# Performance work log

Hardware: AMD Instinct MI355X
Metric: run time of the kernel (lower is better)

## Reference

```python
import jax, jax.numpy as jnp
import numpy as np

NUM_HEADS = 16

def setup_inputs() -> dict:
    key = jax.random.key(0)
    k1, k2, k3 = jax.random.split(key, 3)
    B, S, D = 2, 2048, 1024
    x = jax.random.normal(k1, (B, S, D), dtype=jnp.float32)
    Wqkv = jax.random.normal(k2, (D, 3 * D), dtype=jnp.float32) * (1.0 / np.sqrt(D))
    bqkv = jnp.zeros((3 * D,), dtype=jnp.float32)
    Wo = jax.random.normal(k3, (D, D), dtype=jnp.float32) * (1.0 / np.sqrt(D))
    bo = jnp.zeros((D,), dtype=jnp.float32)
    return {"x": x, "Wqkv": Wqkv, "bqkv": bqkv, "Wo": Wo, "bo": bo}

def reference(x, Wqkv, bqkv, Wo, bo):
    B, S, D = x.shape
    H = NUM_HEADS
    hd = D // H
    # qkv projection, split into per-head q, k, v: [B, H, S, hd]
    qkv = (x @ Wqkv + bqkv).reshape(B, S, H, 3 * hd).transpose(0, 2, 1, 3)
    q, k, v = jnp.split(qkv, 3, axis=-1)
    # causal attention scores [B, H, S, S]
    scores = jnp.einsum('bhqd,bhkd->bhqk', q, k)
    causal = jnp.tril(jnp.ones((S, S), dtype=bool))  # True = keep
    scores = jnp.where(causal, scores, -jnp.inf)
    attn = jax.nn.softmax(scores / np.sqrt(hd).astype(np.float32), axis=-1)
    # dropout is identity in eval mode
    ctx = jnp.einsum('bhqk,bhkd->bhqd', attn, v)  # [B, H, S, hd]
    ctx = ctx.transpose(0, 2, 1, 3).reshape(B, S, D)
    return ctx @ Wo + bo
```

## Files before the change

### kernel.cpp

```cpp
#include <hip/hip_runtime.h>


typedef __attribute__((ext_vector_type(8))) __bf16 bf16x8;
typedef __attribute__((ext_vector_type(4))) float f32x4;
typedef __attribute__((ext_vector_type(4))) short short4v;

__device__ __forceinline__ unsigned short f2bf(float f) {
    union { float f; unsigned u; } v; v.f = f;
    unsigned r = v.u + 0x7fffu + ((v.u >> 16) & 1u);
    return (unsigned short)(r >> 16);
}

__device__ __forceinline__ unsigned pack_bf16x2_trunc(float a, float b) {
#if defined(__HIP_DEVICE_COMPILE__)
    return __builtin_amdgcn_perm(__builtin_bit_cast(unsigned, a),
                                 __builtin_bit_cast(unsigned, b), 0x03020706u);
#else
    return 0u;
#endif
}

__device__ __forceinline__ float fast_exp2(float x) {
#if defined(__HIP_DEVICE_COMPILE__)
    return __builtin_amdgcn_exp2f(x);
#else
    return x;
#endif
}

__device__ __forceinline__ void async_copy16(const unsigned short* g, unsigned short* l) {
    __builtin_amdgcn_global_load_lds(
        (const __attribute__((address_space(1))) unsigned int*)g,
        (__attribute__((address_space(3))) unsigned int*)l, 16, 0, 0);
}

__device__ __forceinline__ f32x4 mfma16x16x16(short4v a, short4v b, f32x4 c) {
#if defined(__HIP_DEVICE_COMPILE__)
    return __builtin_amdgcn_mfma_f32_16x16x16bf16_1k(a, b, c, 0, 0, 0);
#else
    return c;
#endif
}

__global__ __launch_bounds__(256) void convert_f32_bf16(
    const float* __restrict__ in, unsigned short* __restrict__ out)
{
    size_t i = ((size_t)blockIdx.x * 256 + threadIdx.x) * 8;
    float4 v0 = *(const float4*)(in + i);
    float4 v1 = *(const float4*)(in + i + 4);
    ushort4 a, b;
    a.x = f2bf(v0.x); a.y = f2bf(v0.y); a.z = f2bf(v0.z); a.w = f2bf(v0.w);
    b.x = f2bf(v1.x); b.y = f2bf(v1.y); b.z = f2bf(v1.z); b.w = f2bf(v1.w);
    *(ushort4*)(out + i) = a;
    *(ushort4*)(out + i + 4) = b;
}

__global__ __launch_bounds__(256) void transpose_f32_bf16(
    const float* __restrict__ in, unsigned short* __restrict__ out, int K, int N)
{
    __shared__ float T[64][65];
    const int tid = threadIdx.x;
    const int n0 = blockIdx.x * 64, k0 = blockIdx.y * 64;
#pragma unroll
    for (int i = 0; i < 4; i++) {
        int idx = tid + i * 256;
        int r = idx >> 4, c4 = (idx & 15) * 4;
        float4 v = *(const float4*)(in + (size_t)(k0 + r) * N + n0 + c4);
        T[r][c4 + 0] = v.x; T[r][c4 + 1] = v.y; T[r][c4 + 2] = v.z; T[r][c4 + 3] = v.w;
    }
    __syncthreads();
#pragma unroll
    for (int i = 0; i < 4; i++) {
        int idx = tid + i * 256;
        int n = idx >> 4, k4 = (idx & 15) * 4;
        ushort4 o;
        o.x = f2bf(T[k4 + 0][n]); o.y = f2bf(T[k4 + 1][n]);
        o.z = f2bf(T[k4 + 2][n]); o.w = f2bf(T[k4 + 3][n]);
        *(ushort4*)(out + (size_t)(n0 + n) * K + k0 + k4) = o;
    }
}

__global__ __launch_bounds__(256) void transpose_v(
    const unsigned short* __restrict__ vrow, unsigned short* __restrict__ vt)
{
    __shared__ unsigned short T[64 * 72];
    const int tid = threadIdx.x;
    const int bh = blockIdx.y;
    const int s0 = blockIdx.x * 64;
    const unsigned short* src = vrow + ((size_t)bh * 2048 + s0) * 64;
    unsigned short* dst = vt + (size_t)bh * 64 * 2048 + s0;
#pragma unroll
    for (int i = 0; i < 2; i++) {
        int idx = tid + i * 256;
        int s = idx >> 3, dg = (idx & 7) * 8;
        *(uint4*)&T[s * 72 + dg] = *(const uint4*)(src + s * 64 + dg);
    }
    __syncthreads();
#pragma unroll
    for (int i = 0; i < 2; i++) {
        int idx = tid + i * 256;
        int d = idx >> 3, sg = (idx & 7) * 8;
        ushort4 a, b;
        a.x = T[(sg + 0) * 72 + d]; a.y = T[(sg + 1) * 72 + d];
        a.z = T[(sg + 2) * 72 + d]; a.w = T[(sg + 3) * 72 + d];
        b.x = T[(sg + 4) * 72 + d]; b.y = T[(sg + 5) * 72 + d];
        b.z = T[(sg + 6) * 72 + d]; b.w = T[(sg + 7) * 72 + d];
        *(ushort4*)(dst + (size_t)d * 2048 + sg) = a;
        *(ushort4*)(dst + (size_t)d * 2048 + sg + 4) = b;
    }
}

__global__ __launch_bounds__(256) void gemm_qkv_bf(
    const unsigned short* __restrict__ Xbf,
    const unsigned short* __restrict__ WT,
    const float* __restrict__ bias,
    unsigned short* __restrict__ qws, unsigned short* __restrict__ kws,
    unsigned short* __restrict__ vrow)
{
    const int K = 1024;
    __shared__ __align__(16) unsigned short smem[128 * 136];
    unsigned short* As = smem;
    unsigned short* Bs = smem + 8192;
    const int tid = threadIdx.x;
    const int m0 = blockIdx.y * 128, n0 = blockIdx.x * 128;
    const int wave = tid >> 6, lane = tid & 63;
    const int wm = (wave >> 1) * 64, wn = (wave & 1) * 64;
    const int quad = lane >> 4, l16 = lane & 15;
    const int lrow = lane >> 3, lgrp = lane & 7;
    const int sg = lgrp ^ lrow;

    f32x4 acc[4][4];
    const f32x4 Z4 = {0.f, 0.f, 0.f, 0.f};
#pragma unroll
    for (int i = 0; i < 4; i++)
#pragma unroll
        for (int j = 0; j < 4; j++) acc[i][j] = Z4;

    for (int k0 = 0; k0 < K; k0 += 64) {
        __syncthreads();
#pragma unroll
        for (int c = 0; c < 4; c++) {
            int nb = (wave * 4 + c) * 8;
            async_copy16(Xbf + (size_t)(m0 + nb + lrow) * K + k0 + sg * 8, &As[nb * 64]);
            async_copy16(WT  + (size_t)(n0 + nb + lrow) * K + k0 + sg * 8, &Bs[nb * 64]);
        }
        __syncthreads();
#pragma unroll
        for (int kk = 0; kk < 2; kk++) {
            int pg = ((kk * 4 + quad) ^ (l16 & 7)) * 8;
            bf16x8 af[4], bfr[4];
#pragma unroll
            for (int mi = 0; mi < 4; mi++) af[mi] = *(const bf16x8*)&As[(wm + mi * 16 + l16) * 64 + pg];
#pragma unroll
            for (int ni = 0; ni < 4; ni++) bfr[ni] = *(const bf16x8*)&Bs[(wn + ni * 16 + l16) * 64 + pg];
#pragma unroll
            for (int mi = 0; mi < 4; mi++)
#pragma unroll
                for (int ni = 0; ni < 4; ni++)
                    acc[mi][ni] = __builtin_amdgcn_mfma_f32_16x16x32_bf16(af[mi], bfr[ni], acc[mi][ni], 0, 0, 0);
        }
    }
    __syncthreads();
#pragma unroll
    for (int ni = 0; ni < 4; ni++) {
        int colL = wn + ni * 16 + l16;
        int col = n0 + colL;
        int t = (col % 192) >> 6;
        float bv = bias[col];
        float scl = (t == 1) ? 0.18033688f : 1.0f;
#pragma unroll
        for (int mi = 0; mi < 4; mi++)
#pragma unroll
            for (int r = 0; r < 4; r++) {
                int row = wm + mi * 16 + quad * 4 + r;
                smem[row * 136 + colL] = f2bf((acc[mi][ni][r] + bv) * scl);
            }
    }
    __syncthreads();
#pragma unroll
    for (int i = 0; i < 8; i++) {
        int idx = tid + i * 256;
        int row = idx >> 4, g = idx & 15;
        int colL = g * 8;
        uint4 w = *(const uint4*)&smem[row * 136 + colL];
        int col = n0 + colL;
        int h = col / 192, rem = col % 192, t = rem >> 6, d = rem & 63;
        int grow = m0 + row;
        int b = grow >> 11, s = grow & 2047;
        unsigned short* dst = (t == 0) ? qws : (t == 1) ? kws : vrow;
        *(uint4*)(dst + ((size_t)(b * 16 + h) * 2048 + s) * 64 + d) = w;
    }
}

__device__ __constant__ unsigned ATTN_JOBS[47] = {
    16u | (0u<<8) | (17u<<16),
    15u | (0u<<8) | (16u<<16), 30u | (0u<<8) | (16u<<16), 31u | (0u<<8) | (16u<<16), 31u | (16u<<8) | (32u<<16),
    14u | (0u<<8) | (15u<<16), 28u | (0u<<8) | (15u<<16), 29u | (0u<<8) | (15u<<16), 29u | (15u<<8) | (30u<<16), 30u | (16u<<8) | (31u<<16),
    13u | (0u<<8) | (14u<<16), 26u | (0u<<8) | (14u<<16), 27u | (0u<<8) | (14u<<16), 27u | (14u<<8) | (28u<<16), 28u | (15u<<8) | (29u<<16),
    12u | (0u<<8) | (13u<<16), 24u | (0u<<8) | (13u<<16), 25u | (0u<<8) | (13u<<16), 25u | (13u<<8) | (26u<<16), 26u | (14u<<8) | (27u<<16),
    11u | (0u<<8) | (12u<<16), 22u | (0u<<8) | (12u<<16), 23u | (0u<<8) | (12u<<16), 23u | (12u<<8) | (24u<<16), 24u | (13u<<8) | (25u<<16),
    10u | (0u<<8) | (11u<<16), 20u | (0u<<8) | (11u<<16), 21u | (0u<<8) | (11u<<16), 21u | (11u<<8) | (22u<<16), 22u | (12u<<8) | (23u<<16),
     9u | (0u<<8) | (10u<<16), 18u | (0u<<8) | (10u<<16), 19u | (0u<<8) | (10u<<16), 19u | (10u<<8) | (20u<<16), 20u | (11u<<8) | (21u<<16),
     8u | (0u<<8) | ( 9u<<16), 17u | (0u<<8) | ( 9u<<16), 17u | ( 9u<<8) | (18u<<16), 18u | (10u<<8) | (19u<<16),
     7u | (0u<<8) | ( 8u<<16),  6u | (0u<<8) | ( 7u<<16),  5u | (0u<<8) | ( 6u<<16),  4u | (0u<<8) | ( 5u<<16),
     3u | (0u<<8) | ( 4u<<16),  2u | (0u<<8) | ( 3u<<16),  1u | (0u<<8) | ( 2u<<16),  0u | (0u<<8) | ( 1u<<16),
};

__global__ __launch_bounds__(128) void attn(
    const unsigned short* __restrict__ qws, const unsigned short* __restrict__ kws,
    const unsigned short* __restrict__ vtws, unsigned short* __restrict__ ctx,
    unsigned short* __restrict__ Opart, float* __restrict__ lpart)
{
    __shared__ __align__(16) unsigned short Qs[64 * 64];
    __shared__ __align__(16) unsigned short Ks[64 * 64];
    __shared__ __align__(16) unsigned short Vt[64][72];

    const int tid = threadIdx.x;
    const int wave = tid >> 6, lane = tid & 63, quad = lane >> 4, l16 = lane & 15;
    const int lrow = lane >> 3, lgrp = lane & 7;
    const int sg = lgrp ^ lrow;

    const unsigned job = ATTN_JOBS[blockIdx.x >> 5];
    const int bh = blockIdx.x & 31;
    const int tile = job & 0xff;
    const int js = (job >> 8) & 0xff, je = (job >> 16) & 0xff;
    const int q0 = tile * 64;
    const bool split = tile >= 17;

    const unsigned short* Q  = qws + (size_t)bh * 2048 * 64;
    const unsigned short* Kp = kws + (size_t)bh * 2048 * 64;
    const unsigned short* Vp = vtws + (size_t)bh * 64 * 2048;

#pragma unroll
    for (int c = 0; c < 4; c++) {
        int rb = (wave * 4 + c) * 8;
        async_copy16(Q + (size_t)(q0 + rb + lrow) * 64 + sg * 8, &Qs[rb * 64]);
    }

    const int wq = wave * 32;
    f32x4 o[4][2];
    const f32x4 Z4 = {0.f, 0.f, 0.f, 0.f};
#pragma unroll
    for (int dt = 0; dt < 4; dt++)
#pragma unroll
        for (int qt = 0; qt < 2; qt++) o[dt][qt] = Z4;
    float lsum[2] = {0.f, 0.f};

    for (int j = js; j < je; j++) {
        const int kb0 = j * 64;
        __syncthreads();
#pragma unroll
        for (int c = 0; c < 4; c++) {
            int rb = (wave * 4 + c) * 8;
            async_copy16(Kp + (size_t)(kb0 + rb + lrow) * 64 + sg * 8, &Ks[rb * 64]);
        }
#pragma unroll
        for (int ii = 0; ii < 4; ii++) {
            int id2 = tid + ii * 128;
            int row = id2 >> 3, c = (id2 & 7) * 8;
            *(uint4*)&Vt[row][c] = *(const uint4*)(Vp + (size_t)row * 2048 + kb0 + c);
        }
        __syncthreads();

        if (kb0 <= q0 + wq + 31) {
            f32x4 sc[4][2];
#pragma unroll
            for (int kt = 0; kt < 4; kt++)
#pragma unroll
                for (int qt = 0; qt < 2; qt++) sc[kt][qt] = Z4;
#pragma unroll
            for (int kk = 0; kk < 2; kk++) {
                int pg = ((kk * 4 + quad) ^ (l16 & 7)) * 8;
                bf16x8 ak[4], bq[2];
#pragma unroll
                for (int kt = 0; kt < 4; kt++) ak[kt] = *(const bf16x8*)&Ks[(kt * 16 + l16) * 64 + pg];
#pragma unroll
                for (int qt = 0; qt < 2; qt++) bq[qt] = *(const bf16x8*)&Qs[(wq + qt * 16 + l16) * 64 + pg];
#pragma unroll
                for (int kt = 0; kt < 4; kt++)
#pragma unroll
                    for (int qt = 0; qt < 2; qt++)
                        sc[kt][qt] = __builtin_amdgcn_mfma_f32_16x16x32_bf16(ak[kt], bq[qt], sc[kt][qt], 0, 0, 0);
            }
            short4v pb[4][2];
            if (kb0 + 63 <= q0 + wq) {
#pragma unroll
                for (int qt = 0; qt < 2; qt++)
#pragma unroll
                    for (int kt = 0; kt < 4; kt++) {
                        float p0 = fast_exp2(sc[kt][qt][0]);
                        float p1 = fast_exp2(sc[kt][qt][1]);
                        float p2 = fast_exp2(sc[kt][qt][2]);
                        float p3 = fast_exp2(sc[kt][qt][3]);
                        lsum[qt] += (p0 + p1) + (p2 + p3);
                        uint2 uu;
                        uu.x = pack_bf16x2_trunc(p0, p1);
                        uu.y = pack_bf16x2_trunc(p2, p3);
                        pb[kt][qt] = __builtin_bit_cast(short4v, uu);
                    }
            } else {
#pragma unroll
                for (int qt = 0; qt < 2; qt++) {
                    int qg = q0 + wq + qt * 16 + l16;
#pragma unroll
                    for (int kt = 0; kt < 4; kt++) {
                        float p[4];
#pragma unroll
                        for (int r = 0; r < 4; r++) {
                            int key = kb0 + kt * 16 + quad * 4 + r;
                            float t = fast_exp2(sc[kt][qt][r]);
                            p[r] = (key <= qg) ? t : 0.f;
                        }
                        lsum[qt] += (p[0] + p[1]) + (p[2] + p[3]);
                        uint2 uu;
                        uu.x = pack_bf16x2_trunc(p[0], p[1]);
                        uu.y = pack_bf16x2_trunc(p[2], p[3]);
                        pb[kt][qt] = __builtin_bit_cast(short4v, uu);
                    }
                }
            }
#pragma unroll
            for (int kt = 0; kt < 4; kt++) {
#pragma unroll
                for (int dt = 0; dt < 4; dt++) {
                    short4v av = *(const short4v*)&Vt[dt * 16 + l16][kt * 16 + quad * 4];
#pragma unroll
                    for (int qt = 0; qt < 2; qt++)
                        o[dt][qt] = mfma16x16x16(av, pb[kt][qt], o[dt][qt]);
                }
            }
        }
    }
#pragma unroll
    for (int qt = 0; qt < 2; qt++) {
        lsum[qt] += __shfl_xor(lsum[qt], 16);
        lsum[qt] += __shfl_xor(lsum[qt], 32);
    }
    if (!split) {
        const int b = bh >> 4, h = bh & 15;
#pragma unroll
        for (int qt = 0; qt < 2; qt++) {
            int qg = q0 + wq + qt * 16 + l16;
            float inv = 1.0f / lsum[qt];
#pragma unroll
            for (int dt = 0; dt < 4; dt++) {
                ushort4 ov;
                ov.x = f2bf(o[dt][qt][0] * inv);
                ov.y = f2bf(o[dt][qt][1] * inv);
                ov.z = f2bf(o[dt][qt][2] * inv);
                ov.w = f2bf(o[dt][qt][3] * inv);
                *(ushort4*)(ctx + (size_t)(b * 2048 + qg) * 1024 + h * 64 + dt * 16 + quad * 4) = ov;
            }
        }
    } else {
        const int chunk = (js > 0) ? 1 : 0;
        const size_t slot = (size_t)bh * 30 + (tile - 17) * 2 + chunk;
        unsigned short* ob = Opart + slot * 4096;
#pragma unroll
        for (int qt = 0; qt < 2; qt++) {
            int rl = wq + qt * 16 + l16;
#pragma unroll
            for (int dt = 0; dt < 4; dt++) {
                ushort4 ov;
                ov.x = f2bf(o[dt][qt][0]);
                ov.y = f2bf(o[dt][qt][1]);
                ov.z = f2bf(o[dt][qt][2]);
                ov.w = f2bf(o[dt][qt][3]);
                *(ushort4*)(ob + (size_t)rl * 64 + dt * 16 + quad * 4) = ov;
            }
            if (quad == 0) lpart[slot * 64 + rl] = lsum[qt];
        }
    }
}

__global__ __launch_bounds__(256) void attn_combine(
    const unsigned short* __restrict__ Opart, const float* __restrict__ lpart,
    unsigned short* __restrict__ ctx)
{
    const int t = 17 + blockIdx.x;
    const int bh = blockIdx.y;
    const int tid = threadIdx.x;
    const int row = tid >> 2, dg = (tid & 3) * 16;
    const size_t s0 = (size_t)bh * 30 + (t - 17) * 2;
    const float inv = 1.0f / (lpart[s0 * 64 + row] + lpart[(s0 + 1) * 64 + row]);
    const unsigned short* p1 = Opart + s0 * 4096 + (size_t)row * 64 + dg;
    const unsigned short* p2 = p1 + 4096;
    const int b = bh >> 4, h = bh & 15;
    unsigned short* dst = ctx + ((size_t)(b * 2048 + t * 64 + row)) * 1024 + h * 64 + dg;
#pragma unroll
    for (int g = 0; g < 2; g++) {
        ushort a1[8], a2[8], ov[8];
        *(uint4*)a1 = *(const uint4*)(p1 + g * 8);
        *(uint4*)a2 = *(const uint4*)(p2 + g * 8);
#pragma unroll
        for (int e = 0; e < 8; e++) {
            float f1 = __builtin_bit_cast(float, (unsigned)a1[e] << 16);
            float f2 = __builtin_bit_cast(float, (unsigned)a2[e] << 16);
            ov[e] = f2bf((f1 + f2) * inv);
        }
        *(uint4*)(dst + g * 8) = *(const uint4*)ov;
    }
}

__global__ __launch_bounds__(256) void gemm_out(
    const unsigned short* __restrict__ Ctx, const unsigned short* __restrict__ WT,
    const float* __restrict__ bias, float* __restrict__ Out)
{
    const int K = 1024, N = 1024;
    __shared__ __align__(16) unsigned short As[64 * 64];
    __shared__ __align__(16) unsigned short Bs[128 * 64];
    const int tid = threadIdx.x;
    const int m0 = blockIdx.y * 64, n0 = blockIdx.x * 128;
    const int wave = tid >> 6, lane = tid & 63;
    const int wm = (wave >> 1) * 32, wn = (wave & 1) * 64;
    const int quad = lane >> 4, l16 = lane & 15;
    const int lrow = lane >> 3, lgrp = lane & 7;
    const int sg = lgrp ^ lrow;

    f32x4 acc[2][4];
    const f32x4 Z4 = {0.f, 0.f, 0.f, 0.f};
#pragma unroll
    for (int i = 0; i < 2; i++)
#pragma unroll
        for (int j = 0; j < 4; j++) acc[i][j] = Z4;

    for (int k0 = 0; k0 < K; k0 += 64) {
        __syncthreads();
#pragma unroll
        for (int c = 0; c < 2; c++) {
            int nb = (wave * 2 + c) * 8;
            async_copy16(Ctx + (size_t)(m0 + nb + lrow) * K + k0 + sg * 8, &As[nb * 64]);
        }
#pragma unroll
        for (int c = 0; c < 4; c++) {
            int nb = (wave * 4 + c) * 8;
            async_copy16(WT + (size_t)(n0 + nb + lrow) * K + k0 + sg * 8, &Bs[nb * 64]);
        }
        __syncthreads();
#pragma unroll
        for (int kk = 0; kk < 2; kk++) {
            int pg = ((kk * 4 + quad) ^ (l16 & 7)) * 8;
            bf16x8 af[2], bfr[4];
#pragma unroll
            for (int mi = 0; mi < 2; mi++) af[mi] = *(const bf16x8*)&As[(wm + mi * 16 + l16) * 64 + pg];
#pragma unroll
            for (int ni = 0; ni < 4; ni++) bfr[ni] = *(const bf16x8*)&Bs[(wn + ni * 16 + l16) * 64 + pg];
#pragma unroll
            for (int mi = 0; mi < 2; mi++)
#pragma unroll
                for (int ni = 0; ni < 4; ni++)
                    acc[mi][ni] = __builtin_amdgcn_mfma_f32_16x16x32_bf16(af[mi], bfr[ni], acc[mi][ni], 0, 0, 0);
        }
    }
#pragma unroll
    for (int mi = 0; mi < 2; mi++)
#pragma unroll
        for (int ni = 0; ni < 4; ni++) {
            int col = n0 + wn + ni * 16 + l16;
            float bv = bias[col];
#pragma unroll
            for (int r = 0; r < 4; r++) {
                int row = m0 + wm + mi * 16 + quad * 4 + r;
                Out[(size_t)row * N + col] = acc[mi][ni][r] + bv;
            }
        }
}

extern "C" void kernel_launch(void* const* d_in, const int* in_sizes, int n_in,
                              void* d_out, int out_size, void* d_ws, size_t ws_size,
                              hipStream_t stream) {
    const float* x    = (const float*)d_in[0];
    const float* Wqkv = (const float*)d_in[1];
    const float* bqkv = (const float*)d_in[2];
    const float* Wo   = (const float*)d_in[3];
    const float* bo   = (const float*)d_in[4];
    float* out = (float*)d_out;

    const size_t R = 4194304;
    unsigned short* q    = (unsigned short*)d_ws;
    unsigned short* k    = q + R;
    unsigned short* vrow = k + R;
    unsigned short* ctx  = vrow + R;
    unsigned short* xbf  = ctx + R;
    unsigned short* vt   = xbf;
    unsigned short* wqkvT = ctx;
    unsigned short* woT   = q;
    unsigned short* Opart = vrow;
    float* lpart = (float*)(vrow + 960 * (size_t)4096);

    convert_f32_bf16<<<dim3(2048), 256, 0, stream>>>(x, xbf);
    transpose_f32_bf16<<<dim3(48, 16), 256, 0, stream>>>(Wqkv, wqkvT, 1024, 3072);
    gemm_qkv_bf<<<dim3(24, 32), 256, 0, stream>>>(xbf, wqkvT, bqkv, q, k, vrow);
    transpose_v<<<dim3(32, 32), 256, 0, stream>>>(vrow, vt);
    attn<<<dim3(1504), 128, 0, stream>>>(q, k, vt, ctx, Opart, lpart);
    attn_combine<<<dim3(15, 32), 256, 0, stream>>>(Opart, lpart, ctx);
    transpose_f32_bf16<<<dim3(16, 16), 256, 0, stream>>>(Wo, woT, 1024, 1024);
    gemm_out<<<dim3(8, 64), 256, 0, stream>>>(ctx, woT, bo, out);
}
```

Measured before the change: 197.4 us.

## Fuse x fp32-to-bf16 conversion into QKV GEMM and rebalance split-KV attention jobs

Drops the separate conversion kernel: the QKV GEMM now loads fp32 x directly, converts it to bf16 in registers and writes it into swizzled LDS, while the weights still use async global-to-LDS copies. The attention job table is rebuilt so causal query tiles from 12 upward are split into two or three KV chunks. Chunk 0 writes straight into ctx and the combine kernel reads it back, which reduces Opart traffic. In exchange, the GEMM A-tile loads become synchronous and occupy VGPRs, and the combine kernel gains a read-modify-write of ctx.

Measured after the change: 208.0 us. +5.4%, slower.

```diff
diff --git a/kernel.cpp b/kernel.cpp
--- a/kernel.cpp
+++ b/kernel.cpp
@@ -9,6 +9,10 @@
     union { float f; unsigned u; } v; v.f = f;
     unsigned r = v.u + 0x7fffu + ((v.u >> 16) & 1u);
     return (unsigned short)(r >> 16);
+}
+
+__device__ __forceinline__ float bf2f(unsigned short u) {
+    return __builtin_bit_cast(float, (unsigned)u << 16);
 }
 
 __device__ __forceinline__ unsigned pack_bf16x2_trunc(float a, float b) {
@@ -40,19 +44,6 @@
 #else
     return c;
 #endif
-}
-
-__global__ __launch_bounds__(256) void convert_f32_bf16(
-    const float* __restrict__ in, unsigned short* __restrict__ out)
-{
-    size_t i = ((size_t)blockIdx.x * 256 + threadIdx.x) * 8;
-    float4 v0 = *(const float4*)(in + i);
-    float4 v1 = *(const float4*)(in + i + 4);
-    ushort4 a, b;
-    a.x = f2bf(v0.x); a.y = f2bf(v0.y); a.z = f2bf(v0.z); a.w = f2bf(v0.w);
-    b.x = f2bf(v1.x); b.y = f2bf(v1.y); b.z = f2bf(v1.z); b.w = f2bf(v1.w);
-    *(ushort4*)(out + i) = a;
-    *(ushort4*)(out + i + 4) = b;
 }
 
 __global__ __launch_bounds__(256) void transpose_f32_bf16(
@@ -110,8 +101,8 @@
     }
 }
 
-__global__ __launch_bounds__(256) void gemm_qkv_bf(
-    const unsigned short* __restrict__ Xbf,
+__global__ __launch_bounds__(256) void gemm_qkv(
+    const float* __restrict__ X,
     const unsigned short* __restrict__ WT,
     const float* __restrict__ bias,
     unsigned short* __restrict__ qws, unsigned short* __restrict__ kws,
@@ -141,8 +132,21 @@
 #pragma unroll
         for (int c = 0; c < 4; c++) {
             int nb = (wave * 4 + c) * 8;
-            async_copy16(Xbf + (size_t)(m0 + nb + lrow) * K + k0 + sg * 8, &As[nb * 64]);
-            async_copy16(WT  + (size_t)(n0 + nb + lrow) * K + k0 + sg * 8, &Bs[nb * 64]);
+            async_copy16(WT + (size_t)(n0 + nb + lrow) * K + k0 + sg * 8, &Bs[nb * 64]);
+        }
+#pragma unroll
+        for (int i = 0; i < 4; i++) {
+            int idx = tid + i * 256;
+            int m = idx >> 3, g = idx & 7;
+            const float* xp = X + (size_t)(m0 + m) * K + k0 + g * 8;
+            float4 v0 = *(const float4*)xp;
+            float4 v1 = *(const float4*)(xp + 4);
+            ushort4 a, b;
+            a.x = f2bf(v0.x); a.y = f2bf(v0.y); a.z = f2bf(v0.z); a.w = f2bf(v0.w);
+            b.x = f2bf(v1.x); b.y = f2bf(v1.y); b.z = f2bf(v1.z); b.w = f2bf(v1.w);
+            int pg = g ^ (m & 7);
+            *(ushort4*)&As[m * 64 + pg * 8] = a;
+            *(ushort4*)&As[m * 64 + pg * 8 + 4] = b;
         }
         __syncthreads();
 #pragma unroll
@@ -192,19 +196,26 @@
     }
 }
 
-__device__ __constant__ unsigned ATTN_JOBS[47] = {
-    16u | (0u<<8) | (17u<<16),
-    15u | (0u<<8) | (16u<<16), 30u | (0u<<8) | (16u<<16), 31u | (0u<<8) | (16u<<16), 31u | (16u<<8) | (32u<<16),
-    14u | (0u<<8) | (15u<<16), 28u | (0u<<8) | (15u<<16), 29u | (0u<<8) | (15u<<16), 29u | (15u<<8) | (30u<<16), 30u | (16u<<8) | (31u<<16),
-    13u | (0u<<8) | (14u<<16), 26u | (0u<<8) | (14u<<16), 27u | (0u<<8) | (14u<<16), 27u | (14u<<8) | (28u<<16), 28u | (15u<<8) | (29u<<16),
-    12u | (0u<<8) | (13u<<16), 24u | (0u<<8) | (13u<<16), 25u | (0u<<8) | (13u<<16), 25u | (13u<<8) | (26u<<16), 26u | (14u<<8) | (27u<<16),
-    11u | (0u<<8) | (12u<<16), 22u | (0u<<8) | (12u<<16), 23u | (0u<<8) | (12u<<16), 23u | (12u<<8) | (24u<<16), 24u | (13u<<8) | (25u<<16),
-    10u | (0u<<8) | (11u<<16), 20u | (0u<<8) | (11u<<16), 21u | (0u<<8) | (11u<<16), 21u | (11u<<8) | (22u<<16), 22u | (12u<<8) | (23u<<16),
-     9u | (0u<<8) | (10u<<16), 18u | (0u<<8) | (10u<<16), 19u | (0u<<8) | (10u<<16), 19u | (10u<<8) | (20u<<16), 20u | (11u<<8) | (21u<<16),
-     8u | (0u<<8) | ( 9u<<16), 17u | (0u<<8) | ( 9u<<16), 17u | ( 9u<<8) | (18u<<16), 18u | (10u<<8) | (19u<<16),
-     7u | (0u<<8) | ( 8u<<16),  6u | (0u<<8) | ( 7u<<16),  5u | (0u<<8) | ( 6u<<16),  4u | (0u<<8) | ( 5u<<16),
-     3u | (0u<<8) | ( 4u<<16),  2u | (0u<<8) | ( 3u<<16),  1u | (0u<<8) | ( 2u<<16),  0u | (0u<<8) | ( 1u<<16),
+#define J(t, s, e, c) ((unsigned)(t) | ((unsigned)(s) << 8) | ((unsigned)(e) << 16) | ((unsigned)(c) << 24))
+__device__ __constant__ unsigned ATTN_JOBS[60] = {
+    J(22,0,12,0), J(23,0,12,0), J(23,12,24,1), J(11,0,12,0),
+    J(20,0,11,0), J(21,0,11,0), J(21,11,22,1), J(22,12,23,1),
+    J(30,0,11,0), J(31,0,11,0), J(31,11,22,1), J(10,0,11,0),
+    J(18,0,10,0), J(19,0,10,0), J(19,10,20,1), J(20,11,21,1),
+    J(27,0,10,0), J(28,0,10,0), J(28,10,20,1), J(29,0,10,0),
+    J(29,10,20,1), J(29,20,30,2), J(30,11,21,1), J(30,21,31,2),
+    J(31,22,32,2), J(9,0,10,0),
+    J(16,0,9,0), J(17,0,9,0), J(17,9,18,1), J(18,10,19,1),
+    J(24,0,9,0), J(25,0,9,0), J(25,9,18,1), J(26,0,9,0),
+    J(26,9,18,1), J(26,18,27,2), J(27,10,19,1), J(27,19,28,2),
+    J(28,20,29,2), J(8,0,9,0),
+    J(14,0,8,0), J(15,0,8,0), J(15,8,16,1), J(16,9,17,1),
+    J(24,9,17,1), J(24,17,25,2), J(25,18,26,2), J(7,0,8,0),
+    J(12,0,7,0), J(13,0,7,0), J(13,7,14,1), J(14,8,15,1), J(6,0,7,0),
+    J(12,7,13,1), J(5,0,6,0), J(4,0,5,0), J(3,0,4,0), J(2,0,3,0),
+    J(1,0,2,0), J(0,0,1,0),
 };
+#undef J
 
 __global__ __launch_bounds__(128) void attn(
     const unsigned short* __restrict__ qws, const unsigned short* __restrict__ kws,
@@ -224,8 +235,9 @@
     const int bh = blockIdx.x & 31;
     const int tile = job & 0xff;
     const int js = (job >> 8) & 0xff, je = (job >> 16) & 0xff;
+    const int chunk = (job >> 24) & 0xff;
     const int q0 = tile * 64;
-    const bool split = tile >= 17;
+    const bool split = tile >= 12;
 
     const unsigned short* Q  = qws + (size_t)bh * 2048 * 64;
     const unsigned short* Kp = kws + (size_t)bh * 2048 * 64;
@@ -336,8 +348,8 @@
         lsum[qt] += __shfl_xor(lsum[qt], 16);
         lsum[qt] += __shfl_xor(lsum[qt], 32);
     }
+    const int b = bh >> 4, h = bh & 15;
     if (!split) {
-        const int b = bh >> 4, h = bh & 15;
 #pragma unroll
         for (int qt = 0; qt < 2; qt++) {
             int qg = q0 + wq + qt * 16 + l16;
@@ -353,22 +365,45 @@
             }
         }
     } else {
-        const int chunk = (js > 0) ? 1 : 0;
-        const size_t slot = (size_t)bh * 30 + (tile - 17) * 2 + chunk;
-        unsigned short* ob = Opart + slot * 4096;
+        const int ls = (tile < 24) ? (tile - 12) * 2 + chunk
+                                   : 24 + (tile - 24) * 3 + chunk;
+        float* lp = lpart + ((size_t)bh * 48 + ls) * 64;
 #pragma unroll
         for (int qt = 0; qt < 2; qt++) {
             int rl = wq + qt * 16 + l16;
-#pragma unroll
-            for (int dt = 0; dt < 4; dt++) {
-                ushort4 ov;
-                ov.x = f2bf(o[dt][qt][0]);
-                ov.y = f2bf(o[dt][qt][1]);
-                ov.z = f2bf(o[dt][qt][2]);
-                ov.w = f2bf(o[dt][qt][3]);
-                *(ushort4*)(ob + (size_t)rl * 64 + dt * 16 + quad * 4) = ov;
-            }
-            if (quad == 0) lpart[slot * 64 + rl] = lsum[qt];
+            if (quad == 0) lp[rl] = lsum[qt];
+        }
+        if (chunk == 0) {
+#pragma unroll
+            for (int qt = 0; qt < 2; qt++) {
+                int qg = q0 + wq + qt * 16 + l16;
+#pragma unroll
+                for (int dt = 0; dt < 4; dt++) {
+                    ushort4 ov;
+                    ov.x = f2bf(o[dt][qt][0]);
+                    ov.y = f2bf(o[dt][qt][1]);
+                    ov.z = f2bf(o[dt][qt][2]);
+                    ov.w = f2bf(o[dt][qt][3]);
+                    *(ushort4*)(ctx + (size_t)(b * 2048 + qg) * 1024 + h * 64 + dt * 16 + quad * 4) = ov;
+                }
+            }
+        } else {
+            const int os = (tile < 24) ? (tile - 12)
+                                       : 12 + (tile - 24) * 2 + (chunk - 1);
+            unsigned short* ob = Opart + ((size_t)bh * 28 + os) * 4096;
+#pragma unroll
+            for (int qt = 0; qt < 2; qt++) {
+                int rl = wq + qt * 16 + l16;
+#pragma unroll
+                for (int dt = 0; dt < 4; dt++) {
+                    ushort4 ov;
+                    ov.x = f2bf(o[dt][qt][0]);
+                    ov.y = f2bf(o[dt][qt][1]);
+                    ov.z = f2bf(o[dt][qt][2]);
+                    ov.w = f2bf(o[dt][qt][3]);
+                    *(ushort4*)(ob + (size_t)rl * 64 + dt * 16 + quad * 4) = ov;
+                }
+            }
         }
     }
 }
@@ -377,26 +412,31 @@
     const unsigned short* __restrict__ Opart, const float* __restrict__ lpart,
     unsigned short* __restrict__ ctx)
 {
-    const int t = 17 + blockIdx.x;
+    const int t = 12 + blockIdx.x;
     const int bh = blockIdx.y;
     const int tid = threadIdx.x;
     const int row = tid >> 2, dg = (tid & 3) * 16;
-    const size_t s0 = (size_t)bh * 30 + (t - 17) * 2;
-    const float inv = 1.0f / (lpart[s0 * 64 + row] + lpart[(s0 + 1) * 64 + row]);
-    const unsigned short* p1 = Opart + s0 * 4096 + (size_t)row * 64 + dg;
-    const unsigned short* p2 = p1 + 4096;
+    const int nch = (t < 24) ? 2 : 3;
+    const int ls0 = (t < 24) ? (t - 12) * 2 : 24 + (t - 24) * 3;
+    const float* lp = lpart + ((size_t)bh * 48 + ls0) * 64 + row;
+    float lsum = lp[0] + lp[64];
+    if (nch == 3) lsum += lp[128];
+    const float inv = 1.0f / lsum;
+    const int os0 = (t < 24) ? (t - 12) : 12 + (t - 24) * 2;
+    const unsigned short* p1 = Opart + ((size_t)bh * 28 + os0) * 4096 + (size_t)row * 64 + dg;
     const int b = bh >> 4, h = bh & 15;
     unsigned short* dst = ctx + ((size_t)(b * 2048 + t * 64 + row)) * 1024 + h * 64 + dg;
 #pragma unroll
     for (int g = 0; g < 2; g++) {
-        ushort a1[8], a2[8], ov[8];
+        ushort a0[8], a1[8], a2[8], ov[8];
+        *(uint4*)a0 = *(const uint4*)(dst + g * 8);
         *(uint4*)a1 = *(const uint4*)(p1 + g * 8);
-        *(uint4*)a2 = *(const uint4*)(p2 + g * 8);
+        if (nch == 3) *(uint4*)a2 = *(const uint4*)(p1 + 4096 + g * 8);
 #pragma unroll
         for (int e = 0; e < 8; e++) {
-            float f1 = __builtin_bit_cast(float, (unsigned)a1[e] << 16);
-            float f2 = __builtin_bit_cast(float, (unsigned)a2[e] << 16);
-            ov[e] = f2bf((f1 + f2) * inv);
+            float f = bf2f(a0[e]) + bf2f(a1[e]);
+            if (nch == 3) f += bf2f(a2[e]);
+            ov[e] = f2bf(f * inv);
         }
         *(uint4*)(dst + g * 8) = *(const uint4*)ov;
     }
@@ -481,19 +521,17 @@
     unsigned short* k    = q + R;
     unsigned short* vrow = k + R;
     unsigned short* ctx  = vrow + R;
-    unsigned short* xbf  = ctx + R;
-    unsigned short* vt   = xbf;
+    unsigned short* vt   = ctx + R;
     unsigned short* wqkvT = ctx;
     unsigned short* woT   = q;
     unsigned short* Opart = vrow;
-    float* lpart = (float*)(vrow + 960 * (size_t)4096);
-
-    convert_f32_bf16<<<dim3(2048), 256, 0, stream>>>(x, xbf);
+    float* lpart = (float*)(vrow + (size_t)896 * 4096);
+
     transpose_f32_bf16<<<dim3(48, 16), 256, 0, stream>>>(Wqkv, wqkvT, 1024, 3072);
-    gemm_qkv_bf<<<dim3(24, 32), 256, 0, stream>>>(xbf, wqkvT, bqkv, q, k, vrow);
+    gemm_qkv<<<dim3(24, 32), 256, 0, stream>>>(x, wqkvT, bqkv, q, k, vrow);
     transpose_v<<<dim3(32, 32), 256, 0, stream>>>(vrow, vt);
-    attn<<<dim3(1504), 128, 0, stream>>>(q, k, vt, ctx, Opart, lpart);
-    attn_combine<<<dim3(15, 32), 256, 0, stream>>>(Opart, lpart, ctx);
+    attn<<<dim3(1920), 128, 0, stream>>>(q, k, vt, ctx, Opart, lpart);
+    attn_combine<<<dim3(20, 32), 256, 0, stream>>>(Opart, lpart, ctx);
     transpose_f32_bf16<<<dim3(16, 16), 256, 0, stream>>>(Wo, woT, 1024, 1024);
     gemm_out<<<dim3(8, 64), 256, 0, stream>>>(ctx, woT, bo, out);
 }
```
